# Kernel optimization log

Hardware: AMD Instinct MI355X
Metric: run time of the kernel (lower is better)

Reference implementation:

```python
import jax, jax.numpy as jnp
import numpy as np

NUM_HEADS = 16
NUM_KV_HEADS = 4
HEAD_DIM = 128
HALF_DIM = HEAD_DIM // 2
LAMBDA_INIT = 0.8
LAMBDA_MIN = 0.0
LAMBDA_MAX = 1.0
CAUSAL = True
NORMALIZE_DIFF = True
NEG = -1.0e9


def setup_inputs() -> dict:
    key = jax.random.key(0)
    k1, k2, k3 = jax.random.split(key, 3)
    B, Sq, Sk = 1, 2048, 2048
    query = jax.random.normal(k1, (B, NUM_HEADS, Sq, HEAD_DIM), dtype=jnp.float32)
    key_t = jax.random.normal(k2, (B, NUM_KV_HEADS, Sk, HEAD_DIM), dtype=jnp.float32)
    value = jax.random.normal(k3, (B, NUM_KV_HEADS, Sk, HEAD_DIM), dtype=jnp.float32)
    return {"query": query, "key": key_t, "value": value}


def reference(query, key, value):
    scale = 1.0 / (HALF_DIM ** 0.5)
    lam = jnp.clip(jnp.float32(LAMBDA_INIT), LAMBDA_MIN, LAMBDA_MAX)
    # GQA: repeat KV heads to match query heads
    rep = NUM_HEADS // NUM_KV_HEADS
    k = jnp.repeat(key, rep, axis=1)    # [b,h,k,d]
    v = jnp.repeat(value, rep, axis=1)  # [b,h,k,d]
    q1, q2 = query[..., :HALF_DIM], query[..., HALF_DIM:]
    k1, k2 = k[..., :HALF_DIM], k[..., HALF_DIM:]
    scores1 = jnp.einsum('bhqd,bhkd->bhqk', q1, k1) * scale
    scores2 = jnp.einsum('bhqd,bhkd->bhqk', q2, k2) * scale
    if CAUSAL:
        Sq, Sk = query.shape[2], k.shape[2]
        mask = jnp.tril(jnp.ones((Sq, Sk), dtype=jnp.float32))  # lower-triangular causal
        scores1 = scores1 * mask + (1.0 - mask) * NEG
        scores2 = scores2 * mask + (1.0 - mask) * NEG
    attn1 = jax.nn.softmax(scores1, axis=-1)
    attn2 = jax.nn.softmax(scores2, axis=-1)
    diff_attn = attn1 - lam * attn2
    out = jnp.einsum('bhqk,bhkd->bhqd', diff_attn, v)
    if NORMALIZE_DIFF:
        out = out * (1.0 - LAMBDA_INIT)
    return out
```

## Files before the change

kernel.cpp:

```cpp
#include <hip/hip_runtime.h>

#define NUM_HEADS 16
#define HEAD_DIM  128
#define SEQ       2048
#define KT_STRIDE 8192

typedef __attribute__((ext_vector_type(8))) unsigned short us8;
typedef __attribute__((ext_vector_type(8))) __bf16 bf16x8;
typedef __attribute__((ext_vector_type(4))) float f32x4;
typedef __attribute__((ext_vector_type(16))) float f32x16;
typedef __attribute__((ext_vector_type(4))) unsigned u32x4;
typedef __attribute__((ext_vector_type(2))) unsigned u32x2;

static __device__ inline unsigned short f2bf(float x) {
    union { float f; unsigned u; } v; v.f = x;
    unsigned r = v.u + 0x7FFFu + ((v.u >> 16) & 1u);
    return (unsigned short)(r >> 16);
}
static __device__ inline unsigned pk2bf(float a, float b) {
    return (unsigned)f2bf(a) | ((unsigned)f2bf(b) << 16);
}
static __device__ inline float fast_exp2(float x) {
#if __has_builtin(__builtin_amdgcn_exp2f)
    return __builtin_amdgcn_exp2f(x);
#else
    return exp2f(x);
#endif
}
static __device__ inline unsigned pack_hi(unsigned clo, unsigned chi) {
#if __has_builtin(__builtin_amdgcn_perm)
    return __builtin_amdgcn_perm(chi, clo, 0x07060302u);
#else
    return (clo >> 16) | (chi & 0xffff0000u);
#endif
}
static __device__ inline f32x16 mfma32(us8 a, us8 b, f32x16 c) {
    return __builtin_amdgcn_mfma_f32_32x32x16_bf16(
        __builtin_bit_cast(bf16x8, a), __builtin_bit_cast(bf16x8, b), c, 0, 0, 0);
}

__global__ __launch_bounds__(256)
void prep_frag(const float* __restrict__ K, const float* __restrict__ V,
               unsigned short* __restrict__ KF, unsigned short* __restrict__ VF)
{
    const int bx  = (int)blockIdx.x, t = (int)threadIdx.x;
    const int which = bx & 1, khb = (bx >> 1) & 1, kt = (bx >> 2) & 31, kvh = bx >> 7;
    __shared__ __align__(16) float Ls[32][132];

    const float* src = (which ? V : K) + ((size_t)kvh * SEQ + kt * 64 + khb * 32) * HEAD_DIM;
    #pragma unroll
    for (int i = 0; i < 4; ++i) {
        const int idx = t + i * 256;
        const int r = idx >> 5, c4 = idx & 31;
        *(float4*)&Ls[r][c4 * 4] = *(const float4*)(src + (size_t)r * HEAD_DIM + c4 * 4);
    }
    __syncthreads();

    if (!which) {
        #pragma unroll
        for (int i = 0; i < 2; ++i) {
            const int c = t + i * 256;
            const int lane = c & 63, ds = (c >> 6) & 3, mat = (c >> 8) & 1;
            const int H = lane >> 5;
            const int row = lane & 31;
            const int dim = mat * 64 + ds * 16 + H * 8;
            u32x4 pk;
            #pragma unroll
            for (int jj = 0; jj < 4; ++jj)
                pk[jj] = pk2bf(Ls[row][dim + 2*jj], Ls[row][dim + 2*jj + 1]);
            *(us8*)(KF + ((size_t)(kvh * 32 + kt) * 16 + khb * 8 + mat * 4 + ds) * 512 + lane * 8)
                = __builtin_bit_cast(us8, pk);
        }
    } else {
        #pragma unroll
        for (int i = 0; i < 2; ++i) {
            const int c = t + i * 256;
            const int lane = c & 63, db = (c >> 6) & 3, ks = (c >> 8) & 1;
            const int H = lane >> 5;
            const int s0 = ks * 16 + H * 8;
            const int d  = db * 32 + (lane & 31);
            u32x4 pk;
            #pragma unroll
            for (int jj = 0; jj < 4; ++jj)
                pk[jj] = pk2bf(Ls[s0 + 2*jj][d], Ls[s0 + 2*jj + 1][d]);
            *(us8*)(VF + ((size_t)(kvh * 32 + kt) * 16 + khb * 8 + ks * 4 + db) * 512 + lane * 8)
                = __builtin_bit_cast(us8, pk);
        }
    }
}

__global__ __launch_bounds__(256, 3)
void diff_attn_mfma11(const float* __restrict__ Q,
                      const unsigned short* __restrict__ KF,
                      const unsigned short* __restrict__ VF,
                      float* __restrict__ Out)
{
    __shared__ float cb[2][32][136];
    __shared__ float rsb[2][2][32];

    const int t   = (int)threadIdx.x;
    const int wv  = t >> 6;
    const int ln  = t & 63;
    const int mat = wv >> 1;
    const int kh  = wv & 1;
    const int q   = ln & 31;
    const int H   = ln >> 5;

    const int bx  = (int)blockIdx.x;
    const int h   = bx & 15;
    const int qt  = 63 - (bx >> 4);
    const int nkt = (qt >> 1) + 1;
    const int kvh = h >> 2;

    const unsigned short* kfb = KF + ((size_t)kvh * 32 * 16 + kh * 8 + mat * 4) * 512 + ln * 8;
    const unsigned short* vfb = VF + ((size_t)kvh * 32 * 16 + kh * 8) * 512 + ln * 8;

    const float qscale = 0.125f * 1.44269504088896340736f;

    us8 qhi[4];
    auto loadQ = [&](int q0c) {
        const float* qr = Q + ((size_t)h * SEQ + q0c + q) * HEAD_DIM + mat * 64;
        #pragma unroll
        for (int ds = 0; ds < 4; ++ds) {
            const int d0 = ds * 16 + H * 8;
            float x[8];
            *(float4*)&x[0] = *(const float4*)(qr + d0);
            *(float4*)&x[4] = *(const float4*)(qr + d0 + 4);
            us8 hi8;
            #pragma unroll
            for (int j = 0; j < 8; ++j) hi8[j] = f2bf(x[j] * qscale);
            qhi[ds] = hi8;
        }
    };

    f32x16 o[4];
    f32x4  rsv;

    auto epilogue = [&](int q0c) {
        __syncthreads();
        float rsc = (rsv[0] + rsv[1]) + (rsv[2] + rsv[3]);
        rsc += __shfl_xor(rsc, 32, 64);
        if (ln < 32) rsb[mat][kh][ln] = rsc;
        if (kh == 1) {
            #pragma unroll
            for (int db = 0; db < 4; ++db)
                #pragma unroll
                for (int i = 0; i < 4; ++i) {
                    float4 v = { o[db][i*4+0], o[db][i*4+1], o[db][i*4+2], o[db][i*4+3] };
                    *(float4*)&cb[mat][q][db * 32 + 8 * i + 4 * H] = v;
                }
        }
        __syncthreads();
        if (kh == 0) {
            const float l = rsb[mat][0][q] + rsb[mat][1][q];
            const float a = mat ? (0.16f / l) : (0.2f / l);
            #pragma unroll
            for (int db = 0; db < 4; ++db)
                #pragma unroll
                for (int i = 0; i < 4; ++i) {
                    float4 v = *(float4*)&cb[mat][q][db * 32 + 8 * i + 4 * H];
                    o[db][i*4+0] = (o[db][i*4+0] + v.x) * a;
                    o[db][i*4+1] = (o[db][i*4+1] + v.y) * a;
                    o[db][i*4+2] = (o[db][i*4+2] + v.z) * a;
                    o[db][i*4+3] = (o[db][i*4+3] + v.w) * a;
                }
            if (mat == 1) {
                #pragma unroll
                for (int db = 0; db < 4; ++db)
                    #pragma unroll
                    for (int i = 0; i < 4; ++i) {
                        float4 v = { o[db][i*4+0], o[db][i*4+1], o[db][i*4+2], o[db][i*4+3] };
                        *(float4*)&cb[1][q][db * 32 + 8 * i + 4 * H] = v;
                    }
            }
        }
        __syncthreads();
        if (wv == 0) {
            float* ob = Out + ((size_t)h * SEQ + q0c + q) * HEAD_DIM;
            #pragma unroll
            for (int db = 0; db < 4; ++db)
                #pragma unroll
                for (int i = 0; i < 4; ++i) {
                    float4 v = *(float4*)&cb[1][q][db * 32 + 8 * i + 4 * H];
                    float4 r;
                    r.x = o[db][i*4+0] - v.x;
                    r.y = o[db][i*4+1] - v.y;
                    r.z = o[db][i*4+2] - v.z;
                    r.w = o[db][i*4+3] - v.w;
                    *(float4*)(ob + db * 32 + 8 * i + 4 * H) = r;
                }
        }
    };

    auto run_seg = [&](int q0c, int nseg) {
        us8 kaA[4], kaB[4];

        auto body = [&](int j, us8 (&kaIn)[4], us8 (&kaOut)[4]) {
            us8 va[8];
            {
                const unsigned short* vb = vfb + (size_t)j * KT_STRIDE;
                #pragma unroll
                for (int c = 0; c < 8; ++c) va[c] = *(const us8*)(vb + c * 512);
            }
            if (j + 1 < nseg) {
                const unsigned short* kb = kfb + (size_t)(j + 1) * KT_STRIDE;
                #pragma unroll
                for (int ds = 0; ds < 4; ++ds) kaOut[ds] = *(const us8*)(kb + ds * 512);
            }
            f32x16 s = (f32x16)0.f;
            #pragma unroll
            for (int ds = 0; ds < 4; ++ds) s = mfma32(kaIn[ds], qhi[ds], s);

            unsigned c[16];
            if (j == nseg - 1) {
                const int kg0 = j * 64 + kh * 32 + 4 * H;
                const int qg  = q0c + q;
                #pragma unroll
                for (int r = 0; r < 16; ++r) {
                    const int kg = kg0 + (r & 3) + ((r >> 2) << 3);
                    float e = (kg <= qg) ? fast_exp2(s[r]) : 0.f;
                    c[r] = __builtin_bit_cast(unsigned, e);
                }
            } else {
                #pragma unroll
                for (int r = 0; r < 16; ++r)
                    c[r] = __builtin_bit_cast(unsigned, fast_exp2(s[r]));
            }
            #pragma unroll
            for (int ks = 0; ks < 2; ++ks) {
                const unsigned pA = pack_hi(c[8*ks+0], c[8*ks+1]);
                const unsigned pB = pack_hi(c[8*ks+2], c[8*ks+3]);
                const unsigned pC = pack_hi(c[8*ks+4], c[8*ks+5]);
                const unsigned pD = pack_hi(c[8*ks+6], c[8*ks+7]);
                rsv[0] += __builtin_bit_cast(float, pA << 16);
                rsv[1] += __builtin_bit_cast(float, pA & 0xffff0000u);
                rsv[2] += __builtin_bit_cast(float, pB << 16);
                rsv[3] += __builtin_bit_cast(float, pB & 0xffff0000u);
                rsv[0] += __builtin_bit_cast(float, pC << 16);
                rsv[1] += __builtin_bit_cast(float, pC & 0xffff0000u);
                rsv[2] += __builtin_bit_cast(float, pD << 16);
                rsv[3] += __builtin_bit_cast(float, pD & 0xffff0000u);
                u32x4 bw;
#if __has_builtin(__builtin_amdgcn_permlane32_swap)
                u32x2 r02 = __builtin_amdgcn_permlane32_swap(pA, pC, false, false);
                u32x2 r13 = __builtin_amdgcn_permlane32_swap(pB, pD, false, false);
                bw[0] = r02[0]; bw[1] = r13[0]; bw[2] = r02[1]; bw[3] = r13[1];
#else
                const unsigned x1 = H ? pA : pC;
                const unsigned x2 = H ? pB : pD;
                const unsigned t1 = (unsigned)__shfl_xor((int)x1, 32, 64);
                const unsigned t2 = (unsigned)__shfl_xor((int)x2, 32, 64);
                bw[0] = H ? t1 : pA;
                bw[1] = H ? t2 : pB;
                bw[2] = H ? pC : t1;
                bw[3] = H ? pD : t2;
#endif
                const us8 bp = __builtin_bit_cast(us8, bw);
                #pragma unroll
                for (int db = 0; db < 4; ++db)
                    o[db] = mfma32(va[ks * 4 + db], bp, o[db]);
            }
        };

        #pragma unroll
        for (int ds = 0; ds < 4; ++ds) kaA[ds] = *(const us8*)(kfb + ds * 512);

        int j = 0;
        for (; j + 2 <= nseg; j += 2) {
            body(j,     kaA, kaB);
            body(j + 1, kaB, kaA);
        }
        if (j < nseg) body(j, kaA, kaB);
    };

    loadQ(qt * 32);
    #pragma unroll
    for (int i = 0; i < 4; ++i) o[i] = (f32x16)0.f;
    rsv = (f32x4)0.f;
    run_seg(qt * 32, nkt);
    epilogue(qt * 32);
}

extern "C" void kernel_launch(void* const* d_in, const int* in_sizes, int n_in,
                              void* d_out, int out_size, void* d_ws, size_t ws_size,
                              hipStream_t stream) {
    const float* Q = (const float*)d_in[0];
    const float* K = (const float*)d_in[1];
    const float* V = (const float*)d_in[2];
    float* Out = (float*)d_out;

    unsigned short* KF = (unsigned short*)d_ws;
    unsigned short* VF = KF + (size_t)4 * SEQ * HEAD_DIM;

    prep_frag<<<512, 256, 0, stream>>>(K, V, KF, VF);
    diff_attn_mfma11<<<1024, 256, 0, stream>>>(Q, KF, VF, Out);
}
```

Before: 135.2 us.

## Software-pipeline QK MFMA one tile ahead and split exp/PV into halves

```diff
diff --git a/kernel.cpp b/kernel.cpp
--- a/kernel.cpp
+++ b/kernel.cpp
@@ -90,7 +90,7 @@
 }
 
 __global__ __launch_bounds__(256, 3)
-void diff_attn_mfma11(const float* __restrict__ Q,
+void diff_attn_mfma12(const float* __restrict__ Q,
                       const unsigned short* __restrict__ KF,
                       const unsigned short* __restrict__ VF,
                       float* __restrict__ Out)
@@ -116,9 +116,10 @@
     const unsigned short* vfb = VF + ((size_t)kvh * 32 * 16 + kh * 8) * 512 + ln * 8;
 
     const float qscale = 0.125f * 1.44269504088896340736f;
+    const int q0c = qt * 32;
 
     us8 qhi[4];
-    auto loadQ = [&](int q0c) {
+    {
         const float* qr = Q + ((size_t)h * SEQ + q0c + q) * HEAD_DIM + mat * 64;
         #pragma unroll
         for (int ds = 0; ds < 4; ++ds) {
@@ -131,154 +132,201 @@
             for (int j = 0; j < 8; ++j) hi8[j] = f2bf(x[j] * qscale);
             qhi[ds] = hi8;
         }
+    }
+
+    f32x16 o[4];
+    #pragma unroll
+    for (int i = 0; i < 4; ++i) o[i] = (f32x16)0.f;
+    f32x4 rsv = (f32x4)0.f;
+
+    us8 ka[4];
+    f32x16 s;
+
+    #pragma unroll
+    for (int ds = 0; ds < 4; ++ds) ka[ds] = *(const us8*)(kfb + ds * 512);
+    s = (f32x16)0.f;
+    #pragma unroll
+    for (int ds = 0; ds < 4; ++ds) s = mfma32(ka[ds], qhi[ds], s);
+
+    auto body = [&](int j, bool last) {
+        const unsigned short* vb = vfb + (size_t)j * KT_STRIDE;
+        us8 va0[4];
+        #pragma unroll
+        for (int c4 = 0; c4 < 4; ++c4) va0[c4] = *(const us8*)(vb + c4 * 512);
+        if (!last) {
+            const unsigned short* kb = kfb + (size_t)(j + 1) * KT_STRIDE;
+            #pragma unroll
+            for (int ds = 0; ds < 4; ++ds) ka[ds] = *(const us8*)(kb + ds * 512);
+        }
+
+        unsigned c0[8];
+        if (last) {
+            const int kg0 = j * 64 + kh * 32 + 4 * H;
+            const int qg  = q0c + q;
+            #pragma unroll
+            for (int r = 0; r < 8; ++r) {
+                const int kg = kg0 + (r & 3) + ((r >> 2) << 3);
+                float e = (kg <= qg) ? fast_exp2(s[r]) : 0.f;
+                c0[r] = __builtin_bit_cast(unsigned, e);
+            }
+        } else {
+            #pragma unroll
+            for (int r = 0; r < 8; ++r)
+                c0[r] = __builtin_bit_cast(unsigned, fast_exp2(s[r]));
+        }
+        unsigned pA = pack_hi(c0[0], c0[1]);
+        unsigned pB = pack_hi(c0[2], c0[3]);
+        unsigned pC = pack_hi(c0[4], c0[5]);
+        unsigned pD = pack_hi(c0[6], c0[7]);
+        rsv[0] += __builtin_bit_cast(float, pA << 16);
+        rsv[1] += __builtin_bit_cast(float, pA & 0xffff0000u);
+        rsv[2] += __builtin_bit_cast(float, pB << 16);
+        rsv[3] += __builtin_bit_cast(float, pB & 0xffff0000u);
+        rsv[0] += __builtin_bit_cast(float, pC << 16);
+        rsv[1] += __builtin_bit_cast(float, pC & 0xffff0000u);
+        rsv[2] += __builtin_bit_cast(float, pD << 16);
+        rsv[3] += __builtin_bit_cast(float, pD & 0xffff0000u);
+        u32x4 bw;
+#if __has_builtin(__builtin_amdgcn_permlane32_swap)
+        {
+            u32x2 r02 = __builtin_amdgcn_permlane32_swap(pA, pC, false, false);
+            u32x2 r13 = __builtin_amdgcn_permlane32_swap(pB, pD, false, false);
+            bw[0] = r02[0]; bw[1] = r13[0]; bw[2] = r02[1]; bw[3] = r13[1];
+        }
+#else
+        {
+            const unsigned x1 = H ? pA : pC;
+            const unsigned x2 = H ? pB : pD;
+            const unsigned t1 = (unsigned)__shfl_xor((int)x1, 32, 64);
+            const unsigned t2 = (unsigned)__shfl_xor((int)x2, 32, 64);
+            bw[0] = H ? t1 : pA;
+            bw[1] = H ? t2 : pB;
+            bw[2] = H ? pC : t1;
+            bw[3] = H ? pD : t2;
+        }
+#endif
+        us8 bp = __builtin_bit_cast(us8, bw);
+
+        us8 va1[4];
+        #pragma unroll
+        for (int c4 = 0; c4 < 4; ++c4) va1[c4] = *(const us8*)(vb + (4 + c4) * 512);
+
+        #pragma unroll
+        for (int db = 0; db < 4; ++db) o[db] = mfma32(va0[db], bp, o[db]);
+
+        if (last) {
+            const int kg0 = j * 64 + kh * 32 + 4 * H;
+            const int qg  = q0c + q;
+            #pragma unroll
+            for (int r = 8; r < 16; ++r) {
+                const int kg = kg0 + (r & 3) + ((r >> 2) << 3);
+                float e = (kg <= qg) ? fast_exp2(s[r]) : 0.f;
+                c0[r - 8] = __builtin_bit_cast(unsigned, e);
+            }
+        } else {
+            #pragma unroll
+            for (int r = 8; r < 16; ++r)
+                c0[r - 8] = __builtin_bit_cast(unsigned, fast_exp2(s[r]));
+        }
+        pA = pack_hi(c0[0], c0[1]);
+        pB = pack_hi(c0[2], c0[3]);
+        pC = pack_hi(c0[4], c0[5]);
+        pD = pack_hi(c0[6], c0[7]);
+        rsv[0] += __builtin_bit_cast(float, pA << 16);
+        rsv[1] += __builtin_bit_cast(float, pA & 0xffff0000u);
+        rsv[2] += __builtin_bit_cast(float, pB << 16);
+        rsv[3] += __builtin_bit_cast(float, pB & 0xffff0000u);
+        rsv[0] += __builtin_bit_cast(float, pC << 16);
+        rsv[1] += __builtin_bit_cast(float, pC & 0xffff0000u);
+        rsv[2] += __builtin_bit_cast(float, pD << 16);
+        rsv[3] += __builtin_bit_cast(float, pD & 0xffff0000u);
+#if __has_builtin(__builtin_amdgcn_permlane32_swap)
+        {
+            u32x2 r02 = __builtin_amdgcn_permlane32_swap(pA, pC, false, false);
+            u32x2 r13 = __builtin_amdgcn_permlane32_swap(pB, pD, false, false);
+            bw[0] = r02[0]; bw[1] = r13[0]; bw[2] = r02[1]; bw[3] = r13[1];
+        }
+#else
+        {
+            const unsigned x1 = H ? pA : pC;
+            const unsigned x2 = H ? pB : pD;
+            const unsigned t1 = (unsigned)__shfl_xor((int)x1, 32, 64);
+            const unsigned t2 = (unsigned)__shfl_xor((int)x2, 32, 64);
+            bw[0] = H ? t1 : pA;
+            bw[1] = H ? t2 : pB;
+            bw[2] = H ? pC : t1;
+            bw[3] = H ? pD : t2;
+        }
+#endif
+        bp = __builtin_bit_cast(us8, bw);
+        #pragma unroll
+        for (int db = 0; db < 4; ++db) o[db] = mfma32(va1[db], bp, o[db]);
+
+        if (!last) {
+            s = (f32x16)0.f;
+            #pragma unroll
+            for (int ds = 0; ds < 4; ++ds) s = mfma32(ka[ds], qhi[ds], s);
+        }
     };
 
-    f32x16 o[4];
-    f32x4  rsv;
-
-    auto epilogue = [&](int q0c) {
-        __syncthreads();
+    for (int j = 0; j < nkt - 1; ++j) body(j, false);
+    body(nkt - 1, true);
+
+    __syncthreads();
+    {
         float rsc = (rsv[0] + rsv[1]) + (rsv[2] + rsv[3]);
         rsc += __shfl_xor(rsc, 32, 64);
         if (ln < 32) rsb[mat][kh][ln] = rsc;
-        if (kh == 1) {
+    }
+    if (kh == 1) {
+        #pragma unroll
+        for (int db = 0; db < 4; ++db)
+            #pragma unroll
+            for (int i = 0; i < 4; ++i) {
+                float4 v = { o[db][i*4+0], o[db][i*4+1], o[db][i*4+2], o[db][i*4+3] };
+                *(float4*)&cb[mat][q][db * 32 + 8 * i + 4 * H] = v;
+            }
+    }
+    __syncthreads();
+    if (kh == 0) {
+        const float l = rsb[mat][0][q] + rsb[mat][1][q];
+        const float a = mat ? (0.16f / l) : (0.2f / l);
+        #pragma unroll
+        for (int db = 0; db < 4; ++db)
+            #pragma unroll
+            for (int i = 0; i < 4; ++i) {
+                float4 v = *(float4*)&cb[mat][q][db * 32 + 8 * i + 4 * H];
+                o[db][i*4+0] = (o[db][i*4+0] + v.x) * a;
+                o[db][i*4+1] = (o[db][i*4+1] + v.y) * a;
+                o[db][i*4+2] = (o[db][i*4+2] + v.z) * a;
+                o[db][i*4+3] = (o[db][i*4+3] + v.w) * a;
+            }
+        if (mat == 1) {
             #pragma unroll
             for (int db = 0; db < 4; ++db)
                 #pragma unroll
                 for (int i = 0; i < 4; ++i) {
                     float4 v = { o[db][i*4+0], o[db][i*4+1], o[db][i*4+2], o[db][i*4+3] };
-                    *(float4*)&cb[mat][q][db * 32 + 8 * i + 4 * H] = v;
+                    *(float4*)&cb[1][q][db * 32 + 8 * i + 4 * H] = v;
                 }
         }
-        __syncthreads();
-        if (kh == 0) {
-            const float l = rsb[mat][0][q] + rsb[mat][1][q];
-            const float a = mat ? (0.16f / l) : (0.2f / l);
-            #pragma unroll
-            for (int db = 0; db < 4; ++db)
-                #pragma unroll
-                for (int i = 0; i < 4; ++i) {
-                    float4 v = *(float4*)&cb[mat][q][db * 32 + 8 * i + 4 * H];
-                    o[db][i*4+0] = (o[db][i*4+0] + v.x) * a;
-                    o[db][i*4+1] = (o[db][i*4+1] + v.y) * a;
-                    o[db][i*4+2] = (o[db][i*4+2] + v.z) * a;
-                    o[db][i*4+3] = (o[db][i*4+3] + v.w) * a;
-                }
-            if (mat == 1) {
-                #pragma unroll
-                for (int db = 0; db < 4; ++db)
-                    #pragma unroll
-                    for (int i = 0; i < 4; ++i) {
-                        float4 v = { o[db][i*4+0], o[db][i*4+1], o[db][i*4+2], o[db][i*4+3] };
-                        *(float4*)&cb[1][q][db * 32 + 8 * i + 4 * H] = v;
-                    }
-            }
-        }
-        __syncthreads();
-        if (wv == 0) {
-            float* ob = Out + ((size_t)h * SEQ + q0c + q) * HEAD_DIM;
-            #pragma unroll
-            for (int db = 0; db < 4; ++db)
-                #pragma unroll
-                for (int i = 0; i < 4; ++i) {
-                    float4 v = *(float4*)&cb[1][q][db * 32 + 8 * i + 4 * H];
-                    float4 r;
-                    r.x = o[db][i*4+0] - v.x;
-                    r.y = o[db][i*4+1] - v.y;
-                    r.z = o[db][i*4+2] - v.z;
-                    r.w = o[db][i*4+3] - v.w;
-                    *(float4*)(ob + db * 32 + 8 * i + 4 * H) = r;
-                }
-        }
-    };
-
-    auto run_seg = [&](int q0c, int nseg) {
-        us8 kaA[4], kaB[4];
-
-        auto body = [&](int j, us8 (&kaIn)[4], us8 (&kaOut)[4]) {
-            us8 va[8];
-            {
-                const unsigned short* vb = vfb + (size_t)j * KT_STRIDE;
-                #pragma unroll
-                for (int c = 0; c < 8; ++c) va[c] = *(const us8*)(vb + c * 512);
-            }
-            if (j + 1 < nseg) {
-                const unsigned short* kb = kfb + (size_t)(j + 1) * KT_STRIDE;
-                #pragma unroll
-                for (int ds = 0; ds < 4; ++ds) kaOut[ds] = *(const us8*)(kb + ds * 512);
-            }
-            f32x16 s = (f32x16)0.f;
-            #pragma unroll
-            for (int ds = 0; ds < 4; ++ds) s = mfma32(kaIn[ds], qhi[ds], s);
-
-            unsigned c[16];
-            if (j == nseg - 1) {
-                const int kg0 = j * 64 + kh * 32 + 4 * H;
-                const int qg  = q0c + q;
-                #pragma unroll
-                for (int r = 0; r < 16; ++r) {
-                    const int kg = kg0 + (r & 3) + ((r >> 2) << 3);
-                    float e = (kg <= qg) ? fast_exp2(s[r]) : 0.f;
-                    c[r] = __builtin_bit_cast(unsigned, e);
-                }
-            } else {
-                #pragma unroll
-                for (int r = 0; r < 16; ++r)
-                    c[r] = __builtin_bit_cast(unsigned, fast_exp2(s[r]));
-            }
-            #pragma unroll
-            for (int ks = 0; ks < 2; ++ks) {
-                const unsigned pA = pack_hi(c[8*ks+0], c[8*ks+1]);
-                const unsigned pB = pack_hi(c[8*ks+2], c[8*ks+3]);
-                const unsigned pC = pack_hi(c[8*ks+4], c[8*ks+5]);
-                const unsigned pD = pack_hi(c[8*ks+6], c[8*ks+7]);
-                rsv[0] += __builtin_bit_cast(float, pA << 16);
-                rsv[1] += __builtin_bit_cast(float, pA & 0xffff0000u);
-                rsv[2] += __builtin_bit_cast(float, pB << 16);
-                rsv[3] += __builtin_bit_cast(float, pB & 0xffff0000u);
-                rsv[0] += __builtin_bit_cast(float, pC << 16);
-                rsv[1] += __builtin_bit_cast(float, pC & 0xffff0000u);
-                rsv[2] += __builtin_bit_cast(float, pD << 16);
-                rsv[3] += __builtin_bit_cast(float, pD & 0xffff0000u);
-                u32x4 bw;
-#if __has_builtin(__builtin_amdgcn_permlane32_swap)
-                u32x2 r02 = __builtin_amdgcn_permlane32_swap(pA, pC, false, false);
-                u32x2 r13 = __builtin_amdgcn_permlane32_swap(pB, pD, false, false);
-                bw[0] = r02[0]; bw[1] = r13[0]; bw[2] = r02[1]; bw[3] = r13[1];
-#else
-                const unsigned x1 = H ? pA : pC;
-                const unsigned x2 = H ? pB : pD;
-                const unsigned t1 = (unsigned)__shfl_xor((int)x1, 32, 64);
-                const unsigned t2 = (unsigned)__shfl_xor((int)x2, 32, 64);
-                bw[0] = H ? t1 : pA;
-                bw[1] = H ? t2 : pB;
-                bw[2] = H ? pC : t1;
-                bw[3] = H ? pD : t2;
-#endif
-                const us8 bp = __builtin_bit_cast(us8, bw);
-                #pragma unroll
-                for (int db = 0; db < 4; ++db)
-                    o[db] = mfma32(va[ks * 4 + db], bp, o[db]);
-            }
-        };
-
-        #pragma unroll
-        for (int ds = 0; ds < 4; ++ds) kaA[ds] = *(const us8*)(kfb + ds * 512);
-
-        int j = 0;
-        for (; j + 2 <= nseg; j += 2) {
-            body(j,     kaA, kaB);
-            body(j + 1, kaB, kaA);
-        }
-        if (j < nseg) body(j, kaA, kaB);
-    };
-
-    loadQ(qt * 32);
-    #pragma unroll
-    for (int i = 0; i < 4; ++i) o[i] = (f32x16)0.f;
-    rsv = (f32x4)0.f;
-    run_seg(qt * 32, nkt);
-    epilogue(qt * 32);
+    }
+    __syncthreads();
+    if (wv == 0) {
+        float* ob = Out + ((size_t)h * SEQ + q0c + q) * HEAD_DIM;
+        #pragma unroll
+        for (int db = 0; db < 4; ++db)
+            #pragma unroll
+            for (int i = 0; i < 4; ++i) {
+                float4 v = *(float4*)&cb[1][q][db * 32 + 8 * i + 4 * H];
+                float4 r;
+                r.x = o[db][i*4+0] - v.x;
+                r.y = o[db][i*4+1] - v.y;
+                r.z = o[db][i*4+2] - v.z;
+                r.w = o[db][i*4+3] - v.w;
+                *(float4*)(ob + db * 32 + 8 * i + 4 * H) = r;
+            }
+    }
 }
 
 extern "C" void kernel_launch(void* const* d_in, const int* in_sizes, int n_in,
@@ -293,5 +341,5 @@
     unsigned short* VF = KF + (size_t)4 * SEQ * HEAD_DIM;
 
     prep_frag<<<512, 256, 0, stream>>>(K, V, KF, VF);
-    diff_attn_mfma11<<<1024, 256, 0, stream>>>(Q, KF, VF, Out);
-}
+    diff_attn_mfma12<<<1024, 256, 0, stream>>>(Q, KF, VF, Out);
+}
```

Result: faster. 112.3 us (-16.9%).

## Process paired q-tiles per block with balanced causal pairing and XCD-aware mapping

Applied to the files above, without the earlier changes.

```diff
diff --git a/kernel.cpp b/kernel.cpp
--- a/kernel.cpp
+++ b/kernel.cpp
@@ -89,8 +89,8 @@
     }
 }
 
-__global__ __launch_bounds__(256, 3)
-void diff_attn_mfma11(const float* __restrict__ Q,
+__global__ __launch_bounds__(256, 1)
+void diff_attn_mfma14(const float* __restrict__ Q,
                       const unsigned short* __restrict__ KF,
                       const unsigned short* __restrict__ VF,
                       float* __restrict__ Out)
@@ -107,18 +107,24 @@
     const int H   = ln >> 5;
 
     const int bx  = (int)blockIdx.x;
-    const int h   = bx & 15;
-    const int qt  = 63 - (bx >> 4);
-    const int nkt = (qt >> 1) + 1;
-    const int kvh = h >> 2;
+    const int xcd = bx & 7;
+    const int u   = bx >> 3;
+    const int kvh = xcd >> 1;
+    const int h   = kvh * 4 + (u & 3);
+    const int ps  = (u >> 2) | ((xcd & 1) << 3);
 
     const unsigned short* kfb = KF + ((size_t)kvh * 32 * 16 + kh * 8 + mat * 4) * 512 + ln * 8;
     const unsigned short* vfb = VF + ((size_t)kvh * 32 * 16 + kh * 8) * 512 + ln * 8;
 
     const float qscale = 0.125f * 1.44269504088896340736f;
 
-    us8 qhi[4];
-    auto loadQ = [&](int q0c) {
+    us8 qhiA[4], qhiB[4];
+    f32x16 oA[4], oB[4];
+    f32x4  rsvA, rsvB;
+    us8 ka[4];
+    f32x16 sA, sB;
+
+    auto loadQ = [&](int q0c, us8 (&qhi)[4]) {
         const float* qr = Q + ((size_t)h * SEQ + q0c + q) * HEAD_DIM + mat * 64;
         #pragma unroll
         for (int ds = 0; ds < 4; ++ds) {
@@ -133,14 +139,63 @@
         }
     };
 
-    f32x16 o[4];
-    f32x4  rsv;
-
-    auto epilogue = [&](int q0c) {
+    auto make_bp = [&](const f32x16& sv, f32x4& rsv, int rbase, int kg0, int qg,
+                       bool dmask) -> us8 {
+        unsigned c0[8];
+        if (dmask) {
+            #pragma unroll
+            for (int r = 0; r < 8; ++r) {
+                const int ri = rbase + r;
+                const int kg = kg0 + (ri & 3) + ((ri >> 2) << 3);
+                float e = (kg <= qg) ? fast_exp2(sv[ri]) : 0.f;
+                c0[r] = __builtin_bit_cast(unsigned, e);
+            }
+        } else {
+            #pragma unroll
+            for (int r = 0; r < 8; ++r)
+                c0[r] = __builtin_bit_cast(unsigned, fast_exp2(sv[rbase + r]));
+        }
+        const unsigned pA = pack_hi(c0[0], c0[1]);
+        const unsigned pB = pack_hi(c0[2], c0[3]);
+        const unsigned pC = pack_hi(c0[4], c0[5]);
+        const unsigned pD = pack_hi(c0[6], c0[7]);
+        rsv[0] += __builtin_bit_cast(float, pA << 16);
+        rsv[1] += __builtin_bit_cast(float, pA & 0xffff0000u);
+        rsv[2] += __builtin_bit_cast(float, pB << 16);
+        rsv[3] += __builtin_bit_cast(float, pB & 0xffff0000u);
+        rsv[0] += __builtin_bit_cast(float, pC << 16);
+        rsv[1] += __builtin_bit_cast(float, pC & 0xffff0000u);
+        rsv[2] += __builtin_bit_cast(float, pD << 16);
+        rsv[3] += __builtin_bit_cast(float, pD & 0xffff0000u);
+        u32x4 bw;
+#if __has_builtin(__builtin_amdgcn_permlane32_swap)
+        {
+            u32x2 r02 = __builtin_amdgcn_permlane32_swap(pA, pC, false, false);
+            u32x2 r13 = __builtin_amdgcn_permlane32_swap(pB, pD, false, false);
+            bw[0] = r02[0]; bw[1] = r13[0]; bw[2] = r02[1]; bw[3] = r13[1];
+        }
+#else
+        {
+            const unsigned x1 = H ? pA : pC;
+            const unsigned x2 = H ? pB : pD;
+            const unsigned t1 = (unsigned)__shfl_xor((int)x1, 32, 64);
+            const unsigned t2 = (unsigned)__shfl_xor((int)x2, 32, 64);
+            bw[0] = H ? t1 : pA;
+            bw[1] = H ? t2 : pB;
+            bw[2] = H ? pC : t1;
+            bw[3] = H ? pD : t2;
+        }
+#endif
+        return __builtin_bit_cast(us8, bw);
+    };
+
+    auto epilogue = [&](f32x16 (&o)[4], f32x4& rsv, int q0c) {
         __syncthreads();
-        float rsc = (rsv[0] + rsv[1]) + (rsv[2] + rsv[3]);
-        rsc += __shfl_xor(rsc, 32, 64);
-        if (ln < 32) rsb[mat][kh][ln] = rsc;
+        {
+            float rsc = (rsv[0] + rsv[1]) + (rsv[2] + rsv[3]);
+            rsc += __shfl_xor(rsc, 32, 64);
+            if (ln < 32) rsb[mat][kh][ln] = rsc;
+        }
         if (kh == 1) {
             #pragma unroll
             for (int db = 0; db < 4; ++db)
@@ -192,93 +247,77 @@
         }
     };
 
-    auto run_seg = [&](int q0c, int nseg) {
-        us8 kaA[4], kaB[4];
-
-        auto body = [&](int j, us8 (&kaIn)[4], us8 (&kaOut)[4]) {
-            us8 va[8];
-            {
-                const unsigned short* vb = vfb + (size_t)j * KT_STRIDE;
-                #pragma unroll
-                for (int c = 0; c < 8; ++c) va[c] = *(const us8*)(vb + c * 512);
+    auto run_pair = [&](int p) {
+        const int nseg = p + 1;
+        const int q0A  = p * 64, q0B = p * 64 + 32;
+        loadQ(q0A, qhiA);
+        loadQ(q0B, qhiB);
+        #pragma unroll
+        for (int i = 0; i < 4; ++i) { oA[i] = (f32x16)0.f; oB[i] = (f32x16)0.f; }
+        rsvA = (f32x4)0.f;
+        rsvB = (f32x4)0.f;
+
+        us8 vaA[8], vaB[8];
+        #pragma unroll
+        for (int ds = 0; ds < 4; ++ds) ka[ds] = *(const us8*)(kfb + ds * 512);
+        #pragma unroll
+        for (int c4 = 0; c4 < 8; ++c4) vaA[c4] = *(const us8*)(vfb + c4 * 512);
+        sA = (f32x16)0.f;
+        #pragma unroll
+        for (int ds = 0; ds < 4; ++ds) sA = mfma32(ka[ds], qhiA[ds], sA);
+        sB = (f32x16)0.f;
+        #pragma unroll
+        for (int ds = 0; ds < 4; ++ds) sB = mfma32(ka[ds], qhiB[ds], sB);
+
+        auto body = [&](int j, us8 (&vC)[8], us8 (&vN)[8]) {
+            const bool last = (j == nseg - 1);
+            if (!last) {
+                const unsigned short* vb = vfb + (size_t)(j + 1) * KT_STRIDE;
+                #pragma unroll
+                for (int c4 = 0; c4 < 8; ++c4) vN[c4] = *(const us8*)(vb + c4 * 512);
+                const unsigned short* kb = kfb + (size_t)(j + 1) * KT_STRIDE;
+                #pragma unroll
+                for (int ds = 0; ds < 4; ++ds) ka[ds] = *(const us8*)(kb + ds * 512);
             }
-            if (j + 1 < nseg) {
-                const unsigned short* kb = kfb + (size_t)(j + 1) * KT_STRIDE;
-                #pragma unroll
-                for (int ds = 0; ds < 4; ++ds) kaOut[ds] = *(const us8*)(kb + ds * 512);
-            }
-            f32x16 s = (f32x16)0.f;
-            #pragma unroll
-            for (int ds = 0; ds < 4; ++ds) s = mfma32(kaIn[ds], qhi[ds], s);
-
-            unsigned c[16];
-            if (j == nseg - 1) {
-                const int kg0 = j * 64 + kh * 32 + 4 * H;
-                const int qg  = q0c + q;
-                #pragma unroll
-                for (int r = 0; r < 16; ++r) {
-                    const int kg = kg0 + (r & 3) + ((r >> 2) << 3);
-                    float e = (kg <= qg) ? fast_exp2(s[r]) : 0.f;
-                    c[r] = __builtin_bit_cast(unsigned, e);
-                }
-            } else {
-                #pragma unroll
-                for (int r = 0; r < 16; ++r)
-                    c[r] = __builtin_bit_cast(unsigned, fast_exp2(s[r]));
-            }
-            #pragma unroll
-            for (int ks = 0; ks < 2; ++ks) {
-                const unsigned pA = pack_hi(c[8*ks+0], c[8*ks+1]);
-                const unsigned pB = pack_hi(c[8*ks+2], c[8*ks+3]);
-                const unsigned pC = pack_hi(c[8*ks+4], c[8*ks+5]);
-                const unsigned pD = pack_hi(c[8*ks+6], c[8*ks+7]);
-                rsv[0] += __builtin_bit_cast(float, pA << 16);
-                rsv[1] += __builtin_bit_cast(float, pA & 0xffff0000u);
-                rsv[2] += __builtin_bit_cast(float, pB << 16);
-                rsv[3] += __builtin_bit_cast(float, pB & 0xffff0000u);
-                rsv[0] += __builtin_bit_cast(float, pC << 16);
-                rsv[1] += __builtin_bit_cast(float, pC & 0xffff0000u);
-                rsv[2] += __builtin_bit_cast(float, pD << 16);
-                rsv[3] += __builtin_bit_cast(float, pD & 0xffff0000u);
-                u32x4 bw;
-#if __has_builtin(__builtin_amdgcn_permlane32_swap)
-                u32x2 r02 = __builtin_amdgcn_permlane32_swap(pA, pC, false, false);
-                u32x2 r13 = __builtin_amdgcn_permlane32_swap(pB, pD, false, false);
-                bw[0] = r02[0]; bw[1] = r13[0]; bw[2] = r02[1]; bw[3] = r13[1];
-#else
-                const unsigned x1 = H ? pA : pC;
-                const unsigned x2 = H ? pB : pD;
-                const unsigned t1 = (unsigned)__shfl_xor((int)x1, 32, 64);
-                const unsigned t2 = (unsigned)__shfl_xor((int)x2, 32, 64);
-                bw[0] = H ? t1 : pA;
-                bw[1] = H ? t2 : pB;
-                bw[2] = H ? pC : t1;
-                bw[3] = H ? pD : t2;
-#endif
-                const us8 bp = __builtin_bit_cast(us8, bw);
-                #pragma unroll
-                for (int db = 0; db < 4; ++db)
-                    o[db] = mfma32(va[ks * 4 + db], bp, o[db]);
+            const int kg0 = j * 64 + kh * 32 + 4 * H;
+            const int qgA = q0A + q, qgB = q0B + q;
+
+            us8 bp = make_bp(sA, rsvA, 0, kg0, qgA, last);
+            #pragma unroll
+            for (int db = 0; db < 4; ++db) oA[db] = mfma32(vC[db], bp, oA[db]);
+            bp = make_bp(sB, rsvB, 0, kg0, qgB, last);
+            #pragma unroll
+            for (int db = 0; db < 4; ++db) oB[db] = mfma32(vC[db], bp, oB[db]);
+            bp = make_bp(sA, rsvA, 8, kg0, qgA, last);
+            #pragma unroll
+            for (int db = 0; db < 4; ++db) oA[db] = mfma32(vC[4 + db], bp, oA[db]);
+            bp = make_bp(sB, rsvB, 8, kg0, qgB, last);
+            #pragma unroll
+            for (int db = 0; db < 4; ++db) oB[db] = mfma32(vC[4 + db], bp, oB[db]);
+
+            if (!last) {
+                sA = (f32x16)0.f;
+                #pragma unroll
+                for (int ds = 0; ds < 4; ++ds) sA = mfma32(ka[ds], qhiA[ds], sA);
+                sB = (f32x16)0.f;
+                #pragma unroll
+                for (int ds = 0; ds < 4; ++ds) sB = mfma32(ka[ds], qhiB[ds], sB);
             }
         };
 
-        #pragma unroll
-        for (int ds = 0; ds < 4; ++ds) kaA[ds] = *(const us8*)(kfb + ds * 512);
-
         int j = 0;
         for (; j + 2 <= nseg; j += 2) {
-            body(j,     kaA, kaB);
-            body(j + 1, kaB, kaA);
-        }
-        if (j < nseg) body(j, kaA, kaB);
+            body(j,     vaA, vaB);
+            body(j + 1, vaB, vaA);
+        }
+        if (j < nseg) body(j, vaA, vaB);
+
+        epilogue(oA, rsvA, q0A);
+        epilogue(oB, rsvB, q0B);
     };
 
-    loadQ(qt * 32);
-    #pragma unroll
-    for (int i = 0; i < 4; ++i) o[i] = (f32x16)0.f;
-    rsv = (f32x4)0.f;
-    run_seg(qt * 32, nkt);
-    epilogue(qt * 32);
+    run_pair(31 - ps);
+    run_pair(ps);
 }
 
 extern "C" void kernel_launch(void* const* d_in, const int* in_sizes, int n_in,
@@ -293,5 +332,5 @@
     unsigned short* VF = KF + (size_t)4 * SEQ * HEAD_DIM;
 
     prep_frag<<<512, 256, 0, stream>>>(K, V, KF, VF);
-    diff_attn_mfma11<<<1024, 256, 0, stream>>>(Q, KF, VF, Out);
-}
+    diff_attn_mfma14<<<256, 256, 0, stream>>>(Q, KF, VF, Out);
+}
```

Result: slower. 222.1 us (+64.3%).

## Share K/V tiles across two query tiles via LDS double-buffering

Applied to the files above, without the earlier changes.

```diff
diff --git a/kernel.cpp b/kernel.cpp
--- a/kernel.cpp
+++ b/kernel.cpp
@@ -89,31 +89,47 @@
     }
 }
 
-__global__ __launch_bounds__(256, 3)
-void diff_attn_mfma11(const float* __restrict__ Q,
+__global__ __launch_bounds__(512, 2)
+void diff_attn_mfma15(const float* __restrict__ Q,
                       const unsigned short* __restrict__ KF,
                       const unsigned short* __restrict__ VF,
                       float* __restrict__ Out)
 {
-    __shared__ float cb[2][32][136];
-    __shared__ float rsb[2][2][32];
-
-    const int t   = (int)threadIdx.x;
-    const int wv  = t >> 6;
-    const int ln  = t & 63;
-    const int mat = wv >> 1;
-    const int kh  = wv & 1;
-    const int q   = ln & 31;
-    const int H   = ln >> 5;
+    __shared__ __align__(16) unsigned short KV[2][16384];
+    __shared__ float cb[2][2][32][136];
+    __shared__ float rsb[2][2][2][32];
+
+    const int t    = (int)threadIdx.x;
+    const int wv   = t >> 6;
+    const int ln   = t & 63;
+    const int qsel = wv >> 2;
+    const int mat  = (wv >> 1) & 1;
+    const int kh   = wv & 1;
+    const int q    = ln & 31;
+    const int H    = ln >> 5;
 
     const int bx  = (int)blockIdx.x;
-    const int h   = bx & 15;
-    const int qt  = 63 - (bx >> 4);
-    const int nkt = (qt >> 1) + 1;
-    const int kvh = h >> 2;
-
-    const unsigned short* kfb = KF + ((size_t)kvh * 32 * 16 + kh * 8 + mat * 4) * 512 + ln * 8;
-    const unsigned short* vfb = VF + ((size_t)kvh * 32 * 16 + kh * 8) * 512 + ln * 8;
+    const int xcd = bx & 7;
+    const int u   = bx >> 3;
+    const int kvh = xcd >> 1;
+    const int h   = kvh * 4 + (u & 3);
+    const int ss  = (u >> 2) | ((xcd & 1) << 3);
+
+    const unsigned short* sgb = (wv < 4 ? KF : VF)
+        + ((size_t)kvh * 32 * 16 + (wv & 3) * 4) * 512 + ln * 8;
+    auto stage = [&](int jt, int b) {
+        const unsigned short* tb = sgb + (size_t)jt * KT_STRIDE;
+        #pragma unroll
+        for (int i = 0; i < 4; ++i) {
+            __builtin_amdgcn_global_load_lds(
+                (const __attribute__((address_space(1))) unsigned int*)(tb + i * 512),
+                (__attribute__((address_space(3))) unsigned int*)&KV[b][(wv * 4 + i) * 512],
+                16, 0, 0);
+        }
+    };
+
+    const int kbase = (kh * 8 + mat * 4) * 512;
+    const int vbase = (16 + kh * 8) * 512;
 
     const float qscale = 0.125f * 1.44269504088896340736f;
 
@@ -136,29 +152,80 @@
     f32x16 o[4];
     f32x4  rsv;
 
+    auto make_bp = [&](const f32x16& sv, int rbase, int kg0, int qg, bool dmask) -> us8 {
+        unsigned c0[8];
+        if (dmask) {
+            #pragma unroll
+            for (int r = 0; r < 8; ++r) {
+                const int ri = rbase + r;
+                const int kg = kg0 + (ri & 3) + ((ri >> 2) << 3);
+                float e = (kg <= qg) ? fast_exp2(sv[ri]) : 0.f;
+                c0[r] = __builtin_bit_cast(unsigned, e);
+            }
+        } else {
+            #pragma unroll
+            for (int r = 0; r < 8; ++r)
+                c0[r] = __builtin_bit_cast(unsigned, fast_exp2(sv[rbase + r]));
+        }
+        const unsigned pA = pack_hi(c0[0], c0[1]);
+        const unsigned pB = pack_hi(c0[2], c0[3]);
+        const unsigned pC = pack_hi(c0[4], c0[5]);
+        const unsigned pD = pack_hi(c0[6], c0[7]);
+        rsv[0] += __builtin_bit_cast(float, pA << 16);
+        rsv[1] += __builtin_bit_cast(float, pA & 0xffff0000u);
+        rsv[2] += __builtin_bit_cast(float, pB << 16);
+        rsv[3] += __builtin_bit_cast(float, pB & 0xffff0000u);
+        rsv[0] += __builtin_bit_cast(float, pC << 16);
+        rsv[1] += __builtin_bit_cast(float, pC & 0xffff0000u);
+        rsv[2] += __builtin_bit_cast(float, pD << 16);
+        rsv[3] += __builtin_bit_cast(float, pD & 0xffff0000u);
+        u32x4 bw;
+#if __has_builtin(__builtin_amdgcn_permlane32_swap)
+        {
+            u32x2 r02 = __builtin_amdgcn_permlane32_swap(pA, pC, false, false);
+            u32x2 r13 = __builtin_amdgcn_permlane32_swap(pB, pD, false, false);
+            bw[0] = r02[0]; bw[1] = r13[0]; bw[2] = r02[1]; bw[3] = r13[1];
+        }
+#else
+        {
+            const unsigned x1 = H ? pA : pC;
+            const unsigned x2 = H ? pB : pD;
+            const unsigned t1 = (unsigned)__shfl_xor((int)x1, 32, 64);
+            const unsigned t2 = (unsigned)__shfl_xor((int)x2, 32, 64);
+            bw[0] = H ? t1 : pA;
+            bw[1] = H ? t2 : pB;
+            bw[2] = H ? pC : t1;
+            bw[3] = H ? pD : t2;
+        }
+#endif
+        return __builtin_bit_cast(us8, bw);
+    };
+
     auto epilogue = [&](int q0c) {
         __syncthreads();
-        float rsc = (rsv[0] + rsv[1]) + (rsv[2] + rsv[3]);
-        rsc += __shfl_xor(rsc, 32, 64);
-        if (ln < 32) rsb[mat][kh][ln] = rsc;
+        {
+            float rsc = (rsv[0] + rsv[1]) + (rsv[2] + rsv[3]);
+            rsc += __shfl_xor(rsc, 32, 64);
+            if (ln < 32) rsb[qsel][mat][kh][ln] = rsc;
+        }
         if (kh == 1) {
             #pragma unroll
             for (int db = 0; db < 4; ++db)
                 #pragma unroll
                 for (int i = 0; i < 4; ++i) {
                     float4 v = { o[db][i*4+0], o[db][i*4+1], o[db][i*4+2], o[db][i*4+3] };
-                    *(float4*)&cb[mat][q][db * 32 + 8 * i + 4 * H] = v;
+                    *(float4*)&cb[qsel][mat][q][db * 32 + 8 * i + 4 * H] = v;
                 }
         }
         __syncthreads();
         if (kh == 0) {
-            const float l = rsb[mat][0][q] + rsb[mat][1][q];
+            const float l = rsb[qsel][mat][0][q] + rsb[qsel][mat][1][q];
             const float a = mat ? (0.16f / l) : (0.2f / l);
             #pragma unroll
             for (int db = 0; db < 4; ++db)
                 #pragma unroll
                 for (int i = 0; i < 4; ++i) {
-                    float4 v = *(float4*)&cb[mat][q][db * 32 + 8 * i + 4 * H];
+                    float4 v = *(float4*)&cb[qsel][mat][q][db * 32 + 8 * i + 4 * H];
                     o[db][i*4+0] = (o[db][i*4+0] + v.x) * a;
                     o[db][i*4+1] = (o[db][i*4+1] + v.y) * a;
                     o[db][i*4+2] = (o[db][i*4+2] + v.z) * a;
@@ -170,18 +237,18 @@
                     #pragma unroll
                     for (int i = 0; i < 4; ++i) {
                         float4 v = { o[db][i*4+0], o[db][i*4+1], o[db][i*4+2], o[db][i*4+3] };
-                        *(float4*)&cb[1][q][db * 32 + 8 * i + 4 * H] = v;
+                        *(float4*)&cb[qsel][1][q][db * 32 + 8 * i + 4 * H] = v;
                     }
             }
         }
         __syncthreads();
-        if (wv == 0) {
+        if (mat == 0 && kh == 0) {
             float* ob = Out + ((size_t)h * SEQ + q0c + q) * HEAD_DIM;
             #pragma unroll
             for (int db = 0; db < 4; ++db)
                 #pragma unroll
                 for (int i = 0; i < 4; ++i) {
-                    float4 v = *(float4*)&cb[1][q][db * 32 + 8 * i + 4 * H];
+                    float4 v = *(float4*)&cb[qsel][1][q][db * 32 + 8 * i + 4 * H];
                     float4 r;
                     r.x = o[db][i*4+0] - v.x;
                     r.y = o[db][i*4+1] - v.y;
@@ -192,93 +259,56 @@
         }
     };
 
-    auto run_seg = [&](int q0c, int nseg) {
-        us8 kaA[4], kaB[4];
-
-        auto body = [&](int j, us8 (&kaIn)[4], us8 (&kaOut)[4]) {
+    int bufc = 0;
+
+    auto run_pair = [&](int p, int nextp) {
+        const int nseg = p + 1;
+        const int q0   = p * 64 + qsel * 32;
+        loadQ(q0);
+        #pragma unroll
+        for (int i = 0; i < 4; ++i) o[i] = (f32x16)0.f;
+        rsv = (f32x4)0.f;
+
+        for (int j = 0; j < nseg; ++j) {
+            if (j + 1 < nseg)      stage(j + 1, bufc ^ 1);
+            else if (nextp >= 0)   stage(0,     bufc ^ 1);
+
+            const unsigned short* bufp = KV[bufc];
+            us8 kaf[4];
+            #pragma unroll
+            for (int ds = 0; ds < 4; ++ds)
+                kaf[ds] = *(const us8*)&bufp[kbase + ds * 512 + ln * 8];
             us8 va[8];
-            {
-                const unsigned short* vb = vfb + (size_t)j * KT_STRIDE;
-                #pragma unroll
-                for (int c = 0; c < 8; ++c) va[c] = *(const us8*)(vb + c * 512);
-            }
-            if (j + 1 < nseg) {
-                const unsigned short* kb = kfb + (size_t)(j + 1) * KT_STRIDE;
-                #pragma unroll
-                for (int ds = 0; ds < 4; ++ds) kaOut[ds] = *(const us8*)(kb + ds * 512);
-            }
+            #pragma unroll
+            for (int c = 0; c < 8; ++c)
+                va[c] = *(const us8*)&bufp[vbase + c * 512 + ln * 8];
+
             f32x16 s = (f32x16)0.f;
             #pragma unroll
-            for (int ds = 0; ds < 4; ++ds) s = mfma32(kaIn[ds], qhi[ds], s);
-
-            unsigned c[16];
-            if (j == nseg - 1) {
-                const int kg0 = j * 64 + kh * 32 + 4 * H;
-                const int qg  = q0c + q;
-                #pragma unroll
-                for (int r = 0; r < 16; ++r) {
-                    const int kg = kg0 + (r & 3) + ((r >> 2) << 3);
-                    float e = (kg <= qg) ? fast_exp2(s[r]) : 0.f;
-                    c[r] = __builtin_bit_cast(unsigned, e);
-                }
-            } else {
-                #pragma unroll
-                for (int r = 0; r < 16; ++r)
-                    c[r] = __builtin_bit_cast(unsigned, fast_exp2(s[r]));
-            }
-            #pragma unroll
-            for (int ks = 0; ks < 2; ++ks) {
-                const unsigned pA = pack_hi(c[8*ks+0], c[8*ks+1]);
-                const unsigned pB = pack_hi(c[8*ks+2], c[8*ks+3]);
-                const unsigned pC = pack_hi(c[8*ks+4], c[8*ks+5]);
-                const unsigned pD = pack_hi(c[8*ks+6], c[8*ks+7]);
-                rsv[0] += __builtin_bit_cast(float, pA << 16);
-                rsv[1] += __builtin_bit_cast(float, pA & 0xffff0000u);
-                rsv[2] += __builtin_bit_cast(float, pB << 16);
-                rsv[3] += __builtin_bit_cast(float, pB & 0xffff0000u);
-                rsv[0] += __builtin_bit_cast(float, pC << 16);
-                rsv[1] += __builtin_bit_cast(float, pC & 0xffff0000u);
-                rsv[2] += __builtin_bit_cast(float, pD << 16);
-                rsv[3] += __builtin_bit_cast(float, pD & 0xffff0000u);
-                u32x4 bw;
-#if __has_builtin(__builtin_amdgcn_permlane32_swap)
-                u32x2 r02 = __builtin_amdgcn_permlane32_swap(pA, pC, false, false);
-                u32x2 r13 = __builtin_amdgcn_permlane32_swap(pB, pD, false, false);
-                bw[0] = r02[0]; bw[1] = r13[0]; bw[2] = r02[1]; bw[3] = r13[1];
-#else
-                const unsigned x1 = H ? pA : pC;
-                const unsigned x2 = H ? pB : pD;
-                const unsigned t1 = (unsigned)__shfl_xor((int)x1, 32, 64);
-                const unsigned t2 = (unsigned)__shfl_xor((int)x2, 32, 64);
-                bw[0] = H ? t1 : pA;
-                bw[1] = H ? t2 : pB;
-                bw[2] = H ? pC : t1;
-                bw[3] = H ? pD : t2;
-#endif
-                const us8 bp = __builtin_bit_cast(us8, bw);
-                #pragma unroll
-                for (int db = 0; db < 4; ++db)
-                    o[db] = mfma32(va[ks * 4 + db], bp, o[db]);
-            }
-        };
-
-        #pragma unroll
-        for (int ds = 0; ds < 4; ++ds) kaA[ds] = *(const us8*)(kfb + ds * 512);
-
-        int j = 0;
-        for (; j + 2 <= nseg; j += 2) {
-            body(j,     kaA, kaB);
-            body(j + 1, kaB, kaA);
-        }
-        if (j < nseg) body(j, kaA, kaB);
-    };
-
-    loadQ(qt * 32);
-    #pragma unroll
-    for (int i = 0; i < 4; ++i) o[i] = (f32x16)0.f;
-    rsv = (f32x4)0.f;
-    run_seg(qt * 32, nkt);
-    epilogue(qt * 32);
+            for (int ds = 0; ds < 4; ++ds) s = mfma32(kaf[ds], qhi[ds], s);
+
+            const bool last = (j == nseg - 1);
+            const int  kg0  = j * 64 + kh * 32 + 4 * H;
+            const int  qg   = q0 + q;
+
+            us8 bp = make_bp(s, 0, kg0, qg, last);
+            #pragma unroll
+            for (int db = 0; db < 4; ++db) o[db] = mfma32(va[db], bp, o[db]);
+            bp = make_bp(s, 8, kg0, qg, last);
+            #pragma unroll
+            for (int db = 0; db < 4; ++db) o[db] = mfma32(va[4 + db], bp, o[db]);
+
+            __syncthreads();
+            bufc ^= 1;
+        }
+        epilogue(p * 64 + qsel * 32);
+    };
+
+    stage(0, bufc);
+    __syncthreads();
+
+    run_pair(31 - ss, ss);
+    run_pair(ss, -1);
 }
 
 extern "C" void kernel_launch(void* const* d_in, const int* in_sizes, int n_in,
@@ -293,5 +323,5 @@
     unsigned short* VF = KF + (size_t)4 * SEQ * HEAD_DIM;
 
     prep_frag<<<512, 256, 0, stream>>>(K, V, KF, VF);
-    diff_attn_mfma11<<<1024, 256, 0, stream>>>(Q, KF, VF, Out);
-}
+    diff_attn_mfma15<<<256, 512, 0, stream>>>(Q, KF, VF, Out);
+}
```

Result: faster. 117.8 us (-12.8%).
